# Performance work log

Measured on AMD Instinct MI355X. Metric: run time of the kernel, lower is better.

## Reference

```python
import jax, jax.numpy as jnp
import numpy as np

STRIDE, PAD, DIL = 1, 1, 1

def setup_inputs() -> dict:
    key = jax.random.key(0)
    k1, k2, k3, k4, k5 = jax.random.split(key, 5)
    B, C, H, W = 4, 64, 96, 96
    Co, kh, kw = 64, 3, 3
    K = kh * kw
    return {
        "input": jax.random.normal(k1, (B, C, H, W), dtype=jnp.float32),
        "offset": jax.random.normal(k2, (B, 2 * K, H, W), dtype=jnp.float32),
        "mask": jax.random.uniform(k3, (B, K, H, W), dtype=jnp.float32),
        "weight": jax.random.normal(k4, (Co, C, kh, kw), dtype=jnp.float32) * 0.05,
        "bias": jax.random.normal(k5, (Co,), dtype=jnp.float32),
    }


def _dcnv2(input, offset, mask, weight, bias):
    B, C, H, W = input.shape
    Co, Ci, kh, kw = weight.shape
    K = kh * kw
    G = offset.shape[1] // (2 * K)  # deformable groups
    Cg = C // G
    Ho = (H + 2 * PAD - DIL * (kh - 1) - 1) // STRIDE + 1
    Wo = (W + 2 * PAD - DIL * (kw - 1) - 1) // STRIDE + 1

    # offsets stored as (dy, dx) pairs per kernel tap, per group
    off = offset.reshape(B, G, K, 2, Ho, Wo)
    dy, dx = off[:, :, :, 0], off[:, :, :, 1]          # [B,G,K,Ho,Wo]
    m = mask.reshape(B, G, K, Ho, Wo)

    ky = (jnp.arange(K, dtype=jnp.float32) // kw) * DIL
    kx = (jnp.arange(K, dtype=jnp.float32) % kw) * DIL
    by = jnp.arange(Ho, dtype=jnp.float32) * STRIDE - PAD
    bx = jnp.arange(Wo, dtype=jnp.float32) * STRIDE - PAD
    py = dy + ky[None, None, :, None, None] + by[None, None, None, :, None]
    px = dx + kx[None, None, :, None, None] + bx[None, None, None, None, :]

    fy, fx = jnp.floor(py), jnp.floor(px)
    wy, wx = py - fy, px - fx                          # bilinear weights
    iy0, ix0 = fy.astype(jnp.int32), fx.astype(jnp.int32)

    img = input.reshape(B * G, Cg, H * W)

    def gather(iy, ix):
        valid = ((iy >= 0) & (iy < H) & (ix >= 0) & (ix < W)).astype(input.dtype)
        idx = jnp.clip(iy, 0, H - 1) * W + jnp.clip(ix, 0, W - 1)  # [B,G,K,Ho,Wo]
        idxf = idx.reshape(B * G, K * Ho * Wo)
        vals = jax.vmap(lambda a, i: a[:, i])(img, idxf)  # [B*G,Cg,K*Ho*Wo]
        vals = vals.reshape(B, G, Cg, K, Ho, Wo)
        return vals * valid.reshape(B, G, 1, K, Ho, Wo)

    v00 = gather(iy0, ix0)
    v01 = gather(iy0, ix0 + 1)
    v10 = gather(iy0 + 1, ix0)
    v11 = gather(iy0 + 1, ix0 + 1)

    wy_ = wy[:, :, None]  # [B,G,1,K,Ho,Wo]
    wx_ = wx[:, :, None]
    samp = (v00 * (1 - wy_) * (1 - wx_) + v01 * (1 - wy_) * wx_
            + v10 * wy_ * (1 - wx_) + v11 * wy_ * wx_)
    samp = samp * m[:, :, None]                        # modulation

    cols = samp.reshape(B, C, K, Ho, Wo)               # im2col columns
    out = jnp.einsum('bckhw,ock->bohw', cols, weight.reshape(Co, Ci, K))
    return out + bias[None, :, None, None]


def reference(input, offset, mask, weight, bias):
    return _dcnv2(input, offset, mask, weight, bias)
```

## Files before the change

### kernel.cpp

```cpp
#include <hip/hip_runtime.h>

#define Bn  4
#define Cn  64
#define Hn  96
#define Wn  96
#define Con 64
#define Kk  9
#define HW  (Hn*Wn)
#define PIX 16
#define CK  (Cn*Kk)
#define NTILE (HW/PIX)

typedef __attribute__((ext_vector_type(8))) short bf16x8;
typedef __attribute__((ext_vector_type(8))) unsigned short u16x8;
typedef __attribute__((ext_vector_type(4))) float f32x4;

static __device__ __forceinline__ float bf2f(ushort u) {
    return __uint_as_float(((unsigned int)u) << 16);
}
static __device__ __forceinline__ ushort f2bf(float f) {
    unsigned int u = __float_as_uint(f);
    u += 0x7FFFu + ((u >> 16) & 1u);
    return (ushort)(u >> 16);
}

static __device__ __forceinline__ bf16x8 blend8(
    float w00, float w01, float w10, float w11,
    u16x8 g00, u16x8 g01, u16x8 g10, u16x8 g11)
{
    u16x8 r;
    #pragma unroll
    for (int j = 0; j < 8; ++j) {
        const float v = w00 * bf2f(g00[j]) + w01 * bf2f(g01[j])
                      + w10 * bf2f(g10[j]) + w11 * bf2f(g11[j]);
        r[j] = f2bf(v);
    }
    return __builtin_bit_cast(bf16x8, r);
}

__global__ __launch_bounds__(256) void dcnv2_prep(
    const float* __restrict__ in, const float* __restrict__ w,
    ushort* __restrict__ nhwc, ushort* __restrict__ wb2)
{
    const int t = threadIdx.x;
    if (blockIdx.x < 576) {
        __shared__ ushort tile[64][66];
        const int bid = blockIdx.x;
        const int b  = bid / 144;
        const int s0 = (bid % 144) * 64;
        const float* ib = in + (size_t)b * Cn * HW;
        #pragma unroll
        for (int i = 0; i < 16; ++i) {
            const int c = i * 4 + (t >> 6);
            tile[t & 63][c] = f2bf(ib[(size_t)c * HW + s0 + (t & 63)]);
        }
        __syncthreads();
        ushort* ob = nhwc + ((size_t)b * HW + s0) * 64;
        #pragma unroll
        for (int i = 0; i < 16; ++i) {
            const int s = i * 4 + (t >> 6);
            ob[s * 64 + (t & 63)] = tile[s][t & 63];
        }
    } else {
        const int e = (blockIdx.x - 576) * 256 + t;
        if (e < Con * CK) {
            const int j  = e & 7;
            const int l  = (e >> 3) & 63;
            const int sk = e >> 9;
            const int s  = sk / 18;
            const int kk = sk - s * 18;
            const int o  = s * 16 + (l & 15);
            const int ck = kk * 32 + (l >> 4) * 8 + j;
            const int kt = ck >> 6;
            const int c  = ck & 63;
            wb2[e] = f2bf(w[(size_t)o * CK + c * Kk + kt]);
        }
    }
}

__global__ __launch_bounds__(64)
__attribute__((amdgpu_waves_per_eu(2, 4)))
void dcnv2_wave(
    const ushort* __restrict__ nhwc,
    const ushort* __restrict__ wb2,
    const float*  __restrict__ offset,
    const float*  __restrict__ mask,
    const float*  __restrict__ bias,
    float* __restrict__ out)
{
    __shared__ u16x8 stage[512];

    const int lane = threadIdx.x;
    const int orig = blockIdx.x;
    const int tile = (orig & 7) * 288 + (orig >> 3);
    const int b    = tile / NTILE;
    const int t16  = tile % NTILE;
    const int pix0 = t16 * PIX;
    const int ho   = pix0 / Wn;
    const int wo0  = pix0 % Wn;
    const int px   = lane & 15;
    const int q    = lane >> 4;
    const int wo   = wo0 + px;
    const int sp   = ho * Wn + wo;
    const int px8  = lane >> 3;
    const int jj   = lane & 7;

    const float* __restrict__ ob = offset + (size_t)b * 2 * Kk * HW + sp;
    const float* __restrict__ mb = mask   + (size_t)b * Kk * HW + sp;
    float dyv[9], dxv[9], mmv[9];
    #pragma unroll
    for (int k = 0; k < 9; ++k) {
        dyv[k] = ob[(size_t)(2 * k) * HW];
        dxv[k] = ob[(size_t)(2 * k + 1) * HW];
        mmv[k] = mb[(size_t)k * HW];
    }

    const ushort* __restrict__ nb = nhwc + (size_t)b * HW * 64;
    const ushort* __restrict__ wl = wb2 + lane * 8;

    f32x4 acc0 = {0.f,0.f,0.f,0.f}, acc1 = {0.f,0.f,0.f,0.f};
    f32x4 acc2 = {0.f,0.f,0.f,0.f}, acc3 = {0.f,0.f,0.f,0.f};

    #pragma unroll
    for (int k = 0; k < 9; ++k) {
        const float py  = dyv[k] + (float)(k / 3) + (float)(ho - 1);
        const float pxf = dxv[k] + (float)(k % 3) + (float)(wo - 1);
        const float fy = floorf(py), fx = floorf(pxf);
        const int iy0 = (int)fy, ix0 = (int)fx;
        const int iy1 = iy0 + 1, ix1 = ix0 + 1;
        const float wy = py - fy, wx = pxf - fx;
        const float vy0 = (iy0 >= 0 && iy0 < Hn) ? 1.f : 0.f;
        const float vy1 = (iy1 >= 0 && iy1 < Hn) ? 1.f : 0.f;
        const float vx0 = (ix0 >= 0 && ix0 < Wn) ? 1.f : 0.f;
        const float vx1 = (ix1 >= 0 && ix1 < Wn) ? 1.f : 0.f;
        const int cy0 = min(max(iy0, 0), Hn - 1), cy1 = min(max(iy1, 0), Hn - 1);
        const int cx0 = min(max(ix0, 0), Wn - 1), cx1 = min(max(ix1, 0), Wn - 1);
        const float m = mmv[k];
        const float w00 = m * (1.f - wy) * (1.f - wx) * vy0 * vx0;
        const float w01 = m * (1.f - wy) * wx         * vy0 * vx1;
        const float w10 = m * wy         * (1.f - wx) * vy1 * vx0;
        const float w11 = m * wy         * wx         * vy1 * vx1;
        const int ac0 = (cy0 * Wn + cx0) * 64;
        const int ac1 = (cy0 * Wn + cx1) * 64;
        const int ac2 = (cy1 * Wn + cx0) * 64;
        const int ac3 = (cy1 * Wn + cx1) * 64;

        #pragma unroll
        for (int c = 0; c < 4; ++c) {
            const int acc_c = (c == 0) ? ac0 : (c == 1) ? ac1 : (c == 2) ? ac2 : ac3;
            #pragma unroll
            for (int h = 0; h < 2; ++h) {
                const int p    = px8 + h * 8;
                const int base = __shfl(acc_c, p);
                const u16x8 g  = *(const u16x8*)(nb + base + jj * 8);
                const int E    = p * 4 + c;
                stage[E * 8 + (jj ^ (E & 7))] = g;
            }
        }

        const ushort* wk = wl + (size_t)(2 * k) * 512;
        const bf16x8 af0a = *(const bf16x8*)(wk);
        const bf16x8 af0b = *(const bf16x8*)(wk + 512);
        const bf16x8 af1a = *(const bf16x8*)(wk + 18 * 512);
        const bf16x8 af1b = *(const bf16x8*)(wk + 19 * 512);
        const bf16x8 af2a = *(const bf16x8*)(wk + 36 * 512);
        const bf16x8 af2b = *(const bf16x8*)(wk + 37 * 512);
        const bf16x8 af3a = *(const bf16x8*)(wk + 54 * 512);
        const bf16x8 af3b = *(const bf16x8*)(wk + 55 * 512);

        const int E0 = px * 4 + 0, E1 = px * 4 + 1, E2 = px * 4 + 2, E3 = px * 4 + 3;
        const u16x8 ga0 = stage[E0 * 8 + (q ^ (E0 & 7))];
        const u16x8 ga1 = stage[E1 * 8 + (q ^ (E1 & 7))];
        const u16x8 ga2 = stage[E2 * 8 + (q ^ (E2 & 7))];
        const u16x8 ga3 = stage[E3 * 8 + (q ^ (E3 & 7))];
        const u16x8 gb0 = stage[E0 * 8 + ((q + 4) ^ (E0 & 7))];
        const u16x8 gb1 = stage[E1 * 8 + ((q + 4) ^ (E1 & 7))];
        const u16x8 gb2 = stage[E2 * 8 + ((q + 4) ^ (E2 & 7))];
        const u16x8 gb3 = stage[E3 * 8 + ((q + 4) ^ (E3 & 7))];

        const bf16x8 bfa = blend8(w00, w01, w10, w11, ga0, ga1, ga2, ga3);
        const bf16x8 bfb = blend8(w00, w01, w10, w11, gb0, gb1, gb2, gb3);

        acc0 = __builtin_amdgcn_mfma_f32_16x16x32_bf16(af0a, bfa, acc0, 0, 0, 0);
        acc0 = __builtin_amdgcn_mfma_f32_16x16x32_bf16(af0b, bfb, acc0, 0, 0, 0);
        acc1 = __builtin_amdgcn_mfma_f32_16x16x32_bf16(af1a, bfa, acc1, 0, 0, 0);
        acc1 = __builtin_amdgcn_mfma_f32_16x16x32_bf16(af1b, bfb, acc1, 0, 0, 0);
        acc2 = __builtin_amdgcn_mfma_f32_16x16x32_bf16(af2a, bfa, acc2, 0, 0, 0);
        acc2 = __builtin_amdgcn_mfma_f32_16x16x32_bf16(af2b, bfb, acc2, 0, 0, 0);
        acc3 = __builtin_amdgcn_mfma_f32_16x16x32_bf16(af3a, bfa, acc3, 0, 0, 0);
        acc3 = __builtin_amdgcn_mfma_f32_16x16x32_bf16(af3b, bfb, acc3, 0, 0, 0);
    }

    float* __restrict__ op = out + (size_t)b * Con * HW + pix0 + px;
    const int orow = q * 4;
    #pragma unroll
    for (int r = 0; r < 4; ++r)
        op[(size_t)(orow + r) * HW] = acc0[r] + bias[orow + r];
    #pragma unroll
    for (int r = 0; r < 4; ++r)
        op[(size_t)(16 + orow + r) * HW] = acc1[r] + bias[16 + orow + r];
    #pragma unroll
    for (int r = 0; r < 4; ++r)
        op[(size_t)(32 + orow + r) * HW] = acc2[r] + bias[32 + orow + r];
    #pragma unroll
    for (int r = 0; r < 4; ++r)
        op[(size_t)(48 + orow + r) * HW] = acc3[r] + bias[48 + orow + r];
}

__global__ __launch_bounds__(256) void dcnv2_fused(
    const float* __restrict__ input, const float* __restrict__ offset,
    const float* __restrict__ mask, const float* __restrict__ weight,
    const float* __restrict__ bias, float* __restrict__ out)
{
    __shared__ float s_w[PIX*Kk][4];
    __shared__ int   s_a[PIX*Kk][4];
    __shared__ float s_samp[CK*PIX];
    const int t = threadIdx.x, blk = blockIdx.x;
    const int b = blk / NTILE, tile = blk % NTILE;
    const int pix0 = tile * PIX, ho = pix0 / Wn, wo0 = pix0 % Wn;
    if (t < PIX*Kk) {
        const int p = t / Kk, k = t - p*Kk, wo = wo0 + p, sp = ho*Wn + wo;
        const float dy = offset[(size_t)(b*2*Kk + 2*k)*HW + sp];
        const float dx = offset[(size_t)(b*2*Kk + 2*k + 1)*HW + sp];
        const float m  = mask[(size_t)(b*Kk + k)*HW + sp];
        const float py = dy + (float)(k/3) + (float)(ho - 1);
        const float px = dx + (float)(k%3) + (float)(wo - 1);
        const float fy = floorf(py), fx = floorf(px);
        const int iy0 = (int)fy, ix0 = (int)fx, iy1 = iy0+1, ix1 = ix0+1;
        const float wy = py - fy, wx = px - fx;
        const float vy0 = (iy0>=0 && iy0<Hn)?1.f:0.f, vy1 = (iy1>=0 && iy1<Hn)?1.f:0.f;
        const float vx0 = (ix0>=0 && ix0<Wn)?1.f:0.f, vx1 = (ix1>=0 && ix1<Wn)?1.f:0.f;
        const int cy0 = min(max(iy0,0),Hn-1), cy1 = min(max(iy1,0),Hn-1);
        const int cx0 = min(max(ix0,0),Wn-1), cx1 = min(max(ix1,0),Wn-1);
        s_w[t][0]=m*(1.f-wy)*(1.f-wx)*vy0*vx0; s_w[t][1]=m*(1.f-wy)*wx*vy0*vx1;
        s_w[t][2]=m*wy*(1.f-wx)*vy1*vx0;       s_w[t][3]=m*wy*wx*vy1*vx1;
        s_a[t][0]=cy0*Wn+cx0; s_a[t][1]=cy0*Wn+cx1; s_a[t][2]=cy1*Wn+cx0; s_a[t][3]=cy1*Wn+cx1;
    }
    __syncthreads();
    {
        const float* inb = input + (size_t)b*Cn*HW;
        #pragma unroll 4
        for (int e = t; e < CK*PIX; e += 256) {
            const int ck = e >> 4, p = e & 15, c = ck / 9, k = ck - c*9, pk = p*Kk + k;
            const float* ic = inb + (size_t)c*HW;
            s_samp[ck*PIX + p] = s_w[pk][0]*ic[s_a[pk][0]] + s_w[pk][1]*ic[s_a[pk][1]]
                               + s_w[pk][2]*ic[s_a[pk][2]] + s_w[pk][3]*ic[s_a[pk][3]];
        }
    }
    __syncthreads();
    const int o = t & 63, pg = t >> 6;
    const float4* wrow = (const float4*)(weight + (size_t)o*CK);
    float ax=0.f, ay=0.f, az=0.f, aw=0.f;
    #pragma unroll 4
    for (int qq = 0; qq < CK/4; ++qq) {
        const float4 wv = wrow[qq];
        const float4 s0 = *(const float4*)&s_samp[(4*qq+0)*PIX + pg*4];
        const float4 s1 = *(const float4*)&s_samp[(4*qq+1)*PIX + pg*4];
        const float4 s2 = *(const float4*)&s_samp[(4*qq+2)*PIX + pg*4];
        const float4 s3 = *(const float4*)&s_samp[(4*qq+3)*PIX + pg*4];
        ax += wv.x*s0.x + wv.y*s1.x + wv.z*s2.x + wv.w*s3.x;
        ay += wv.x*s0.y + wv.y*s1.y + wv.z*s2.y + wv.w*s3.y;
        az += wv.x*s0.z + wv.y*s1.z + wv.z*s2.z + wv.w*s3.z;
        aw += wv.x*s0.w + wv.y*s1.w + wv.z*s2.w + wv.w*s3.w;
    }
    const float bo = bias[o];
    float* op = out + (size_t)(b*Con + o)*HW + pix0 + pg*4;
    op[0]=ax+bo; op[1]=ay+bo; op[2]=az+bo; op[3]=aw+bo;
}

extern "C" void kernel_launch(void* const* d_in, const int* in_sizes, int n_in,
                              void* d_out, int out_size, void* d_ws, size_t ws_size,
                              hipStream_t stream) {
    const float* input  = (const float*)d_in[0];
    const float* offset = (const float*)d_in[1];
    const float* mask   = (const float*)d_in[2];
    const float* weight = (const float*)d_in[3];
    const float* bias   = (const float*)d_in[4];
    float* out = (float*)d_out;

    const size_t nhwc_bytes = (size_t)Bn * HW * 64 * 2;
    const size_t wb_bytes   = (size_t)Con * CK * 2;
    if (ws_size >= nhwc_bytes + wb_bytes) {
        ushort* nhwc = (ushort*)d_ws;
        ushort* wbuf = (ushort*)((char*)d_ws + nhwc_bytes);
        hipLaunchKernelGGL(dcnv2_prep, dim3(720), dim3(256), 0, stream,
                           input, weight, nhwc, wbuf);
        hipLaunchKernelGGL(dcnv2_wave, dim3(Bn * NTILE), dim3(64), 0, stream,
                           nhwc, wbuf, offset, mask, bias, out);
    } else {
        hipLaunchKernelGGL(dcnv2_fused, dim3(Bn * NTILE), dim3(256), 0, stream,
                           input, offset, mask, weight, bias, out);
    }
}
```

Before: 28.72 us.

## Process two output rows per wave to reuse weight fragments across tiles

Measured after the change: 32.46 us. 1.13x slower.

```diff
diff --git a/kernel.cpp b/kernel.cpp
--- a/kernel.cpp
+++ b/kernel.cpp
@@ -79,7 +79,7 @@
 }
 
 __global__ __launch_bounds__(64)
-__attribute__((amdgpu_waves_per_eu(2, 4)))
+__attribute__((amdgpu_waves_per_eu(1, 2)))
 void dcnv2_wave(
     const ushort* __restrict__ nhwc,
     const ushort* __restrict__ wb2,
@@ -88,73 +88,85 @@
     const float*  __restrict__ bias,
     float* __restrict__ out)
 {
-    __shared__ u16x8 stage[512];
+    __shared__ u16x8 stage[2][512];
 
     const int lane = threadIdx.x;
     const int orig = blockIdx.x;
-    const int tile = (orig & 7) * 288 + (orig >> 3);
-    const int b    = tile / NTILE;
-    const int t16  = tile % NTILE;
-    const int pix0 = t16 * PIX;
-    const int ho   = pix0 / Wn;
-    const int wo0  = pix0 % Wn;
+    const int pair = (orig & 7) * 144 + (orig >> 3);
+    const int b    = pair / 288;
+    const int pp   = pair % 288;
+    const int ho0  = (pp / 6) * 2;
+    const int wo0  = (pp % 6) * 16;
     const int px   = lane & 15;
     const int q    = lane >> 4;
-    const int wo   = wo0 + px;
-    const int sp   = ho * Wn + wo;
     const int px8  = lane >> 3;
     const int jj   = lane & 7;
-
-    const float* __restrict__ ob = offset + (size_t)b * 2 * Kk * HW + sp;
-    const float* __restrict__ mb = mask   + (size_t)b * Kk * HW + sp;
-    float dyv[9], dxv[9], mmv[9];
+    const int fpx  = px & 7;
+    const int wo   = wo0 + px;
+
+    float dyv[2][9], dxv[2][9], mmv[2][9];
+    #pragma unroll
+    for (int h = 0; h < 2; ++h) {
+        const int sp = (ho0 + h) * Wn + wo;
+        const float* __restrict__ ob = offset + (size_t)b * 2 * Kk * HW + sp;
+        const float* __restrict__ mb = mask   + (size_t)b * Kk * HW + sp;
+        #pragma unroll
+        for (int k = 0; k < 9; ++k) {
+            dyv[h][k] = ob[(size_t)(2 * k) * HW];
+            dxv[h][k] = ob[(size_t)(2 * k + 1) * HW];
+            mmv[h][k] = mb[(size_t)k * HW];
+        }
+    }
+
+    const ushort* __restrict__ nb = nhwc + (size_t)b * HW * 64;
+    const ushort* __restrict__ wl = wb2 + lane * 8;
+
+    f32x4 acc0_0 = {0,0,0,0}, acc0_1 = {0,0,0,0}, acc0_2 = {0,0,0,0}, acc0_3 = {0,0,0,0};
+    f32x4 acc1_0 = {0,0,0,0}, acc1_1 = {0,0,0,0}, acc1_2 = {0,0,0,0}, acc1_3 = {0,0,0,0};
+
     #pragma unroll
     for (int k = 0; k < 9; ++k) {
-        dyv[k] = ob[(size_t)(2 * k) * HW];
-        dxv[k] = ob[(size_t)(2 * k + 1) * HW];
-        mmv[k] = mb[(size_t)k * HW];
-    }
-
-    const ushort* __restrict__ nb = nhwc + (size_t)b * HW * 64;
-    const ushort* __restrict__ wl = wb2 + lane * 8;
-
-    f32x4 acc0 = {0.f,0.f,0.f,0.f}, acc1 = {0.f,0.f,0.f,0.f};
-    f32x4 acc2 = {0.f,0.f,0.f,0.f}, acc3 = {0.f,0.f,0.f,0.f};
-
-    #pragma unroll
-    for (int k = 0; k < 9; ++k) {
-        const float py  = dyv[k] + (float)(k / 3) + (float)(ho - 1);
-        const float pxf = dxv[k] + (float)(k % 3) + (float)(wo - 1);
-        const float fy = floorf(py), fx = floorf(pxf);
-        const int iy0 = (int)fy, ix0 = (int)fx;
-        const int iy1 = iy0 + 1, ix1 = ix0 + 1;
-        const float wy = py - fy, wx = pxf - fx;
-        const float vy0 = (iy0 >= 0 && iy0 < Hn) ? 1.f : 0.f;
-        const float vy1 = (iy1 >= 0 && iy1 < Hn) ? 1.f : 0.f;
-        const float vx0 = (ix0 >= 0 && ix0 < Wn) ? 1.f : 0.f;
-        const float vx1 = (ix1 >= 0 && ix1 < Wn) ? 1.f : 0.f;
-        const int cy0 = min(max(iy0, 0), Hn - 1), cy1 = min(max(iy1, 0), Hn - 1);
-        const int cx0 = min(max(ix0, 0), Wn - 1), cx1 = min(max(ix1, 0), Wn - 1);
-        const float m = mmv[k];
-        const float w00 = m * (1.f - wy) * (1.f - wx) * vy0 * vx0;
-        const float w01 = m * (1.f - wy) * wx         * vy0 * vx1;
-        const float w10 = m * wy         * (1.f - wx) * vy1 * vx0;
-        const float w11 = m * wy         * wx         * vy1 * vx1;
-        const int ac0 = (cy0 * Wn + cx0) * 64;
-        const int ac1 = (cy0 * Wn + cx1) * 64;
-        const int ac2 = (cy1 * Wn + cx0) * 64;
-        const int ac3 = (cy1 * Wn + cx1) * 64;
-
-        #pragma unroll
-        for (int c = 0; c < 4; ++c) {
-            const int acc_c = (c == 0) ? ac0 : (c == 1) ? ac1 : (c == 2) ? ac2 : ac3;
+        float w00[2], w01[2], w10[2], w11[2];
+        int ac0[2], ac1[2], ac2[2], ac3[2];
+        #pragma unroll
+        for (int h = 0; h < 2; ++h) {
+            const int ho = ho0 + h;
+            const float py  = dyv[h][k] + (float)(k / 3) + (float)(ho - 1);
+            const float pxf = dxv[h][k] + (float)(k % 3) + (float)(wo - 1);
+            const float fy = floorf(py), fx = floorf(pxf);
+            const int iy0 = (int)fy, ix0 = (int)fx;
+            const int iy1 = iy0 + 1, ix1 = ix0 + 1;
+            const float wy = py - fy, wx = pxf - fx;
+            const float vy0 = (iy0 >= 0 && iy0 < Hn) ? 1.f : 0.f;
+            const float vy1 = (iy1 >= 0 && iy1 < Hn) ? 1.f : 0.f;
+            const float vx0 = (ix0 >= 0 && ix0 < Wn) ? 1.f : 0.f;
+            const float vx1 = (ix1 >= 0 && ix1 < Wn) ? 1.f : 0.f;
+            const int cy0 = min(max(iy0, 0), Hn - 1), cy1 = min(max(iy1, 0), Hn - 1);
+            const int cx0 = min(max(ix0, 0), Wn - 1), cx1 = min(max(ix1, 0), Wn - 1);
+            const float m = mmv[h][k];
+            w00[h] = m * (1.f - wy) * (1.f - wx) * vy0 * vx0;
+            w01[h] = m * (1.f - wy) * wx         * vy0 * vx1;
+            w10[h] = m * wy         * (1.f - wx) * vy1 * vx0;
+            w11[h] = m * wy         * wx         * vy1 * vx1;
+            ac0[h] = (cy0 * Wn + cx0) * 64;
+            ac1[h] = (cy0 * Wn + cx1) * 64;
+            ac2[h] = (cy1 * Wn + cx0) * 64;
+            ac3[h] = (cy1 * Wn + cx1) * 64;
+        }
+
+        #pragma unroll
+        for (int h = 0; h < 2; ++h) {
             #pragma unroll
-            for (int h = 0; h < 2; ++h) {
-                const int p    = px8 + h * 8;
-                const int base = __shfl(acc_c, p);
-                const u16x8 g  = *(const u16x8*)(nb + base + jj * 8);
-                const int E    = p * 4 + c;
-                stage[E * 8 + (jj ^ (E & 7))] = g;
+            for (int c = 0; c < 4; ++c) {
+                const int a = (c == 0) ? ac0[h] : (c == 1) ? ac1[h]
+                            : (c == 2) ? ac2[h] : ac3[h];
+                #pragma unroll
+                for (int hh = 0; hh < 2; ++hh) {
+                    const int p    = px8 + hh * 8;
+                    const int base = __shfl(a, p);
+                    const u16x8 g  = *(const u16x8*)(nb + base + jj * 8);
+                    stage[h][(p * 4 + c) * 8 + (jj ^ (p & 7))] = g;
+                }
             }
         }
 
@@ -168,43 +180,64 @@
         const bf16x8 af3a = *(const bf16x8*)(wk + 54 * 512);
         const bf16x8 af3b = *(const bf16x8*)(wk + 55 * 512);
 
-        const int E0 = px * 4 + 0, E1 = px * 4 + 1, E2 = px * 4 + 2, E3 = px * 4 + 3;
-        const u16x8 ga0 = stage[E0 * 8 + (q ^ (E0 & 7))];
-        const u16x8 ga1 = stage[E1 * 8 + (q ^ (E1 & 7))];
-        const u16x8 ga2 = stage[E2 * 8 + (q ^ (E2 & 7))];
-        const u16x8 ga3 = stage[E3 * 8 + (q ^ (E3 & 7))];
-        const u16x8 gb0 = stage[E0 * 8 + ((q + 4) ^ (E0 & 7))];
-        const u16x8 gb1 = stage[E1 * 8 + ((q + 4) ^ (E1 & 7))];
-        const u16x8 gb2 = stage[E2 * 8 + ((q + 4) ^ (E2 & 7))];
-        const u16x8 gb3 = stage[E3 * 8 + ((q + 4) ^ (E3 & 7))];
-
-        const bf16x8 bfa = blend8(w00, w01, w10, w11, ga0, ga1, ga2, ga3);
-        const bf16x8 bfb = blend8(w00, w01, w10, w11, gb0, gb1, gb2, gb3);
-
-        acc0 = __builtin_amdgcn_mfma_f32_16x16x32_bf16(af0a, bfa, acc0, 0, 0, 0);
-        acc0 = __builtin_amdgcn_mfma_f32_16x16x32_bf16(af0b, bfb, acc0, 0, 0, 0);
-        acc1 = __builtin_amdgcn_mfma_f32_16x16x32_bf16(af1a, bfa, acc1, 0, 0, 0);
-        acc1 = __builtin_amdgcn_mfma_f32_16x16x32_bf16(af1b, bfb, acc1, 0, 0, 0);
-        acc2 = __builtin_amdgcn_mfma_f32_16x16x32_bf16(af2a, bfa, acc2, 0, 0, 0);
-        acc2 = __builtin_amdgcn_mfma_f32_16x16x32_bf16(af2b, bfb, acc2, 0, 0, 0);
-        acc3 = __builtin_amdgcn_mfma_f32_16x16x32_bf16(af3a, bfa, acc3, 0, 0, 0);
-        acc3 = __builtin_amdgcn_mfma_f32_16x16x32_bf16(af3b, bfb, acc3, 0, 0, 0);
-    }
-
-    float* __restrict__ op = out + (size_t)b * Con * HW + pix0 + px;
+        #pragma unroll
+        for (int h = 0; h < 2; ++h) {
+            const int E0 = px * 4 + 0, E1 = px * 4 + 1, E2 = px * 4 + 2, E3 = px * 4 + 3;
+            const u16x8 ga0 = stage[h][E0 * 8 + (q ^ fpx)];
+            const u16x8 ga1 = stage[h][E1 * 8 + (q ^ fpx)];
+            const u16x8 ga2 = stage[h][E2 * 8 + (q ^ fpx)];
+            const u16x8 ga3 = stage[h][E3 * 8 + (q ^ fpx)];
+            const u16x8 gb0 = stage[h][E0 * 8 + ((q + 4) ^ fpx)];
+            const u16x8 gb1 = stage[h][E1 * 8 + ((q + 4) ^ fpx)];
+            const u16x8 gb2 = stage[h][E2 * 8 + ((q + 4) ^ fpx)];
+            const u16x8 gb3 = stage[h][E3 * 8 + ((q + 4) ^ fpx)];
+
+            const bf16x8 bfa = blend8(w00[h], w01[h], w10[h], w11[h], ga0, ga1, ga2, ga3);
+            const bf16x8 bfb = blend8(w00[h], w01[h], w10[h], w11[h], gb0, gb1, gb2, gb3);
+
+            if (h == 0) {
+                acc0_0 = __builtin_amdgcn_mfma_f32_16x16x32_bf16(af0a, bfa, acc0_0, 0, 0, 0);
+                acc0_0 = __builtin_amdgcn_mfma_f32_16x16x32_bf16(af0b, bfb, acc0_0, 0, 0, 0);
+                acc0_1 = __builtin_amdgcn_mfma_f32_16x16x32_bf16(af1a, bfa, acc0_1, 0, 0, 0);
+                acc0_1 = __builtin_amdgcn_mfma_f32_16x16x32_bf16(af1b, bfb, acc0_1, 0, 0, 0);
+                acc0_2 = __builtin_amdgcn_mfma_f32_16x16x32_bf16(af2a, bfa, acc0_2, 0, 0, 0);
+                acc0_2 = __builtin_amdgcn_mfma_f32_16x16x32_bf16(af2b, bfb, acc0_2, 0, 0, 0);
+                acc0_3 = __builtin_amdgcn_mfma_f32_16x16x32_bf16(af3a, bfa, acc0_3, 0, 0, 0);
+                acc0_3 = __builtin_amdgcn_mfma_f32_16x16x32_bf16(af3b, bfb, acc0_3, 0, 0, 0);
+            } else {
+                acc1_0 = __builtin_amdgcn_mfma_f32_16x16x32_bf16(af0a, bfa, acc1_0, 0, 0, 0);
+                acc1_0 = __builtin_amdgcn_mfma_f32_16x16x32_bf16(af0b, bfb, acc1_0, 0, 0, 0);
+                acc1_1 = __builtin_amdgcn_mfma_f32_16x16x32_bf16(af1a, bfa, acc1_1, 0, 0, 0);
+                acc1_1 = __builtin_amdgcn_mfma_f32_16x16x32_bf16(af1b, bfb, acc1_1, 0, 0, 0);
+                acc1_2 = __builtin_amdgcn_mfma_f32_16x16x32_bf16(af2a, bfa, acc1_2, 0, 0, 0);
+                acc1_2 = __builtin_amdgcn_mfma_f32_16x16x32_bf16(af2b, bfb, acc1_2, 0, 0, 0);
+                acc1_3 = __builtin_amdgcn_mfma_f32_16x16x32_bf16(af3a, bfa, acc1_3, 0, 0, 0);
+                acc1_3 = __builtin_amdgcn_mfma_f32_16x16x32_bf16(af3b, bfb, acc1_3, 0, 0, 0);
+            }
+        }
+    }
+
     const int orow = q * 4;
     #pragma unroll
-    for (int r = 0; r < 4; ++r)
-        op[(size_t)(orow + r) * HW] = acc0[r] + bias[orow + r];
-    #pragma unroll
-    for (int r = 0; r < 4; ++r)
-        op[(size_t)(16 + orow + r) * HW] = acc1[r] + bias[16 + orow + r];
-    #pragma unroll
-    for (int r = 0; r < 4; ++r)
-        op[(size_t)(32 + orow + r) * HW] = acc2[r] + bias[32 + orow + r];
-    #pragma unroll
-    for (int r = 0; r < 4; ++r)
-        op[(size_t)(48 + orow + r) * HW] = acc3[r] + bias[48 + orow + r];
+    for (int h = 0; h < 2; ++h) {
+        float* __restrict__ op = out + (size_t)b * Con * HW + (ho0 + h) * Wn + wo0 + px;
+        const f32x4 a0 = h ? acc1_0 : acc0_0;
+        const f32x4 a1 = h ? acc1_1 : acc0_1;
+        const f32x4 a2 = h ? acc1_2 : acc0_2;
+        const f32x4 a3 = h ? acc1_3 : acc0_3;
+        #pragma unroll
+        for (int r = 0; r < 4; ++r)
+            op[(size_t)(orow + r) * HW] = a0[r] + bias[orow + r];
+        #pragma unroll
+        for (int r = 0; r < 4; ++r)
+            op[(size_t)(16 + orow + r) * HW] = a1[r] + bias[16 + orow + r];
+        #pragma unroll
+        for (int r = 0; r < 4; ++r)
+            op[(size_t)(32 + orow + r) * HW] = a2[r] + bias[32 + orow + r];
+        #pragma unroll
+        for (int r = 0; r < 4; ++r)
+            op[(size_t)(48 + orow + r) * HW] = a3[r] + bias[48 + orow + r];
+    }
 }
 
 __global__ __launch_bounds__(256) void dcnv2_fused(
@@ -285,7 +318,7 @@
         ushort* wbuf = (ushort*)((char*)d_ws + nhwc_bytes);
         hipLaunchKernelGGL(dcnv2_prep, dim3(720), dim3(256), 0, stream,
                            input, weight, nhwc, wbuf);
-        hipLaunchKernelGGL(dcnv2_wave, dim3(Bn * NTILE), dim3(64), 0, stream,
+        hipLaunchKernelGGL(dcnv2_wave, dim3(Bn * 288), dim3(64), 0, stream,
                            nhwc, wbuf, offset, mask, bias, out);
     } else {
         hipLaunchKernelGGL(dcnv2_fused, dim3(Bn * NTILE), dim3(256), 0, stream,
```
